# Performance work log

Measured on AMD Instinct MI355X. Metric: run time of the kernel, lower is better.

## Reference

```python
import jax, jax.numpy as jnp
import numpy as np

CUTOFF = 5.0
NUM_RBF = 8
POLY_P = 5
AVG_NEIGH = 16.0
NUM_LAYERS = 2
NUM_RANKS = 4  # edge angular ranks 0..3 (Cartesian dims 1,3,9,27)
C = 64


def _radial(edge_vec):
    # r: [E,1]; Bessel-j0 basis with polynomial cutoff envelope (MACE-style)
    r = jnp.sqrt(jnp.sum(edge_vec * edge_vec, axis=-1, keepdims=True) + 1e-12)
    x = r / CUTOFF
    p = float(POLY_P)
    env = (1.0 - 0.5 * (p + 1.0) * (p + 2.0) * x**POLY_P
           + p * (p + 2.0) * x**(POLY_P + 1)
           - 0.5 * p * (p + 1.0) * x**(POLY_P + 2))
    env = jnp.where(x < 1.0, env, 0.0)
    k = jnp.arange(1, NUM_RBF + 1, dtype=edge_vec.dtype)
    basis = jnp.sqrt(2.0 / CUTOFF) * jnp.sin(k * jnp.pi * x) / r  # [E,K]
    return basis * env, r


def _angular(rhat):
    # Cartesian ICTD-style angular basis, ranks 0..3, norm constants sqrt(2r+1)
    E = rhat.shape[0]
    y0 = jnp.ones((E, 1), rhat.dtype)
    y1 = jnp.sqrt(3.0) * rhat  # [E,3]
    o2 = rhat[:, :, None] * rhat[:, None, :]
    y2 = jnp.sqrt(5.0) * o2.reshape(E, 9)
    o3 = o2[:, :, :, None] * rhat[:, None, None, :]
    y3 = jnp.sqrt(7.0) * o3.reshape(E, 27)
    return (y0, y1, y2, y3)


def setup_inputs() -> dict:
    key = jax.random.key(0)
    ks = jax.random.split(key, 12)
    N, E = 5000, 80000
    species = jax.random.randint(ks[0], (N,), 0, 10, dtype=jnp.int32)
    senders = jax.random.randint(ks[1], (E,), 0, N, dtype=jnp.int32)
    receivers = jax.random.randint(ks[2], (E,), 0, N, dtype=jnp.int32)
    edge_vec = 1.5 * jax.random.normal(ks[3], (E, 3), jnp.float32)
    embed_w = jax.random.normal(ks[4], (10, C), jnp.float32)
    rad_w1 = jax.random.normal(ks[5], (NUM_LAYERS, NUM_RBF, 64), jnp.float32) / np.sqrt(NUM_RBF)
    rad_w2 = jax.random.normal(ks[6], (NUM_LAYERS, 64, 64), jnp.float32) / 8.0
    rad_w3 = jax.random.normal(ks[7], (NUM_LAYERS, 64, 64), jnp.float32) / 8.0
    rad_w4 = jax.random.normal(ks[8], (NUM_LAYERS, 64, NUM_RANKS * C), jnp.float32) / 8.0
    mix_w = jax.random.normal(ks[9], (NUM_LAYERS, NUM_RANKS, C, C), jnp.float32) / 8.0
    read_w = jax.random.normal(ks[10], (NUM_LAYERS, C), jnp.float32) / 8.0
    return {"species": species, "senders": senders, "receivers": receivers,
            "edge_vec": edge_vec, "embed_w": embed_w, "rad_w1": rad_w1,
            "rad_w2": rad_w2, "rad_w3": rad_w3, "rad_w4": rad_w4,
            "mix_w": mix_w, "read_w": read_w}


def reference(species, senders, receivers, edge_vec, embed_w,
              rad_w1, rad_w2, rad_w3, rad_w4, mix_w, read_w):
    N = species.shape[0]
    E = edge_vec.shape[0]
    rb, r = _radial(edge_vec)                      # [E,K]
    rhat = edge_vec / r
    Y = _angular(rhat)                             # tuple of [E,dim_r]
    h0 = embed_w[species]                          # [N,C] species embedding
    node_energy = jnp.zeros((N,), edge_vec.dtype)
    for l in range(NUM_LAYERS):
        # radial MLP -> per-rank, per-channel edge weights [E, NUM_RANKS, C]
        h = jax.nn.silu(rb @ rad_w1[l])
        h = jax.nn.silu(h @ rad_w2[l])
        h = jax.nn.silu(h @ rad_w3[l])
        R = (h @ rad_w4[l]).reshape(E, NUM_RANKS, C)
        hj = h0[senders]                           # neighbor gather [E,C]
        h0_new = jnp.zeros_like(h0)
        for ri in range(NUM_RANKS):
            # equivariant edge tensor product: radial * scalar feat x angular
            m = (R[:, ri, :] * hj)[:, :, None] * Y[ri][:, None, :]  # [E,C,dim]
            A = jax.ops.segment_sum(m, receivers, num_segments=N) / AVG_NEIGH
            if ri == 0:
                h0_new = h0_new + A[..., 0] @ mix_w[l, 0]
            else:
                # correlation-2 invariant contraction of equivariant features
                h0_new = h0_new + jnp.einsum('ncd,ncd->nc', A, A) @ mix_w[l, ri]
        node_energy = node_energy + h0_new @ read_w[l]
        h0 = h0_new
    return node_energy
```

## Files before the change

kernel.cpp:

```cpp
#include <hip/hip_runtime.h>
#include <math.h>


#define PI_F 3.14159265358979323846f
#define LOG2E_F 1.44269504088896340736f

typedef _Float16 f16x8 __attribute__((ext_vector_type(8)));
typedef _Float16 f16x2 __attribute__((ext_vector_type(2)));
typedef float f32x4 __attribute__((ext_vector_type(4)));

union FU { uint4 u; f16x8 h; };

__device__ __forceinline__ float silu_f(float x) {
    float e = __builtin_amdgcn_exp2f(-LOG2E_F * x);
    return x * __builtin_amdgcn_rcpf(1.0f + e);
}

__device__ __forceinline__ uint pack2_f16(float a, float b) {
    return __builtin_bit_cast(uint, __builtin_amdgcn_cvt_pkrtz(a, b));
}

__device__ __forceinline__ float unpk_f16(uint u, int hi) {
    unsigned short s = hi ? (unsigned short)(u >> 16) : (unsigned short)(u & 0xffff);
    return (float)__builtin_bit_cast(_Float16, s);
}

__global__ void k_edge_basis(const float* __restrict__ ev,
                             const int* __restrict__ recv,
                             uint*  __restrict__ rbh,
                             float* __restrict__ rhat4,
                             int*   __restrict__ counts,
                             int E)
{
    int e = blockIdx.x * blockDim.x + threadIdx.x;
    if (e >= E) return;
    float vx = ev[3*e+0], vy = ev[3*e+1], vz = ev[3*e+2];
    float r2 = vx*vx + vy*vy + vz*vz + 1e-12f;
    float r  = sqrtf(r2);
    float x  = r * 0.2f;
    float x2 = x*x;
    float x5 = x2*x2*x;
    float env = 1.0f + x5*(-21.0f + x*(35.0f - 15.0f*x));
    if (x >= 1.0f) env = 0.0f;
    float pref = 0.632455532033675866f / r * env;
    float pix  = PI_F * x;
    float bas[8];
    #pragma unroll
    for (int k = 0; k < 8; ++k) bas[k] = pref * __sinf((float)(k+1) * pix);
    uint* o = rbh + (size_t)e*4;
    #pragma unroll
    for (int k = 0; k < 4; ++k) o[k] = pack2_f16(bas[2*k], bas[2*k+1]);

    float ir = 1.0f / r;
    float4 rh;
    rh.x = vx*ir; rh.y = vy*ir; rh.z = vz*ir; rh.w = 0.0f;
    *(float4*)(rhat4 + (size_t)e*4) = rh;

    atomicAdd(&counts[recv[e]], 1);
}

__global__ void k_scan(const int* __restrict__ counts, int* __restrict__ offsets, int N)
{
    __shared__ int wsum[16];
    __shared__ int basev;
    int lane = threadIdx.x & 63;
    int w    = threadIdx.x >> 6;
    if (threadIdx.x == 0) basev = 0;
    __syncthreads();
    for (int start = 0; start < N; start += 1024) {
        int i = start + (int)threadIdx.x;
        int v = (i < N) ? counts[i] : 0;
        int s = v;
        #pragma unroll
        for (int off = 1; off < 64; off <<= 1) {
            int t = __shfl_up(s, off, 64);
            if (lane >= off) s += t;
        }
        if (lane == 63) wsum[w] = s;
        __syncthreads();
        int wbase = 0;
        {
            int ws = (lane < 16) ? wsum[lane] : 0;
            #pragma unroll
            for (int off = 1; off < 16; off <<= 1) {
                int t = __shfl_up(ws, off, 64);
                if (lane >= off) ws += t;
            }
            int excl = __shfl(ws, w - 1, 64);
            wbase = (w == 0) ? 0 : excl;
        }
        if (i < N) offsets[i] = basev + wbase + s - v;
        __syncthreads();
        if (threadIdx.x == 1023) basev += wbase + s;
        __syncthreads();
    }
    if (threadIdx.x == 0) offsets[N] = basev;
}

__global__ void k_scatter(const int* __restrict__ recv,
                          const int* __restrict__ offsets,
                          int* __restrict__ cursor,
                          int* __restrict__ elist, int E)
{
    int e = blockIdx.x * blockDim.x + threadIdx.x;
    if (e >= E) return;
    int r = recv[e];
    int p = atomicAdd(&cursor[r], 1);
    elist[offsets[r] + p] = e;
}

__global__ __launch_bounds__(256) void k_sort_wave(
    const int* __restrict__ offsets, int* __restrict__ elist, int N)
{
    int lane = threadIdx.x & 63;
    int node = (blockIdx.x * blockDim.x + threadIdx.x) >> 6;
    if (node >= N) return;
    int beg = offsets[node], end = offsets[node+1];
    int d = end - beg;
    if (d <= 1) return;
    if (d <= 64) {
        int v = (lane < d) ? elist[beg + lane] : 0x7fffffff;
        int rank = 0;
        #pragma unroll 8
        for (int j = 0; j < 64; ++j) {
            int vj = __shfl(v, j, 64);
            rank += (vj < v) ? 1 : 0;
        }
        if (lane < d) elist[beg + rank] = v;
    } else {
        if (lane == 0) {
            for (int i = beg + 1; i < end; ++i) {
                int v = elist[i];
                int j = i - 1;
                while (j >= beg && elist[j] > v) { elist[j+1] = elist[j]; --j; }
                elist[j+1] = v;
            }
        }
    }
}

__global__ void k_embed(const int* __restrict__ species,
                        const float* __restrict__ embw,
                        float* __restrict__ h0, int NC)
{
    int i = blockIdx.x * blockDim.x + threadIdx.x;
    if (i >= NC) return;
    int n = i >> 6, c = i & 63;
    h0[i] = embw[species[n]*64 + c];
}

__global__ void k_prep_w(const float* __restrict__ rw1,
                         const float* __restrict__ rw2,
                         const float* __restrict__ rw3,
                         const float* __restrict__ rw4,
                         uint* __restrict__ Wf1, uint* __restrict__ Wf2,
                         uint* __restrict__ Wf3, uint* __restrict__ Wf4)
{
    int tid = blockIdx.x * blockDim.x + threadIdx.x;
    if (tid < 2048) {
        int reg = tid & 3, lane = (tid >> 2) & 63, ot = (tid >> 8) & 3, l = tid >> 10;
        int out = 16*ot + (lane & 15);
        int k   = 8*(lane >> 4) + 2*reg;
        float lo = (k   < 8) ? rw1[l*512 + k*64 + out]     : 0.0f;
        float hi = (k+1 < 8) ? rw1[l*512 + (k+1)*64 + out] : 0.0f;
        Wf1[tid] = pack2_f16(lo, hi);
        return;
    }
    int t = tid - 2048;
    if (t < 4096) {
        int reg = t & 3, lane = (t >> 2) & 63, kt = (t >> 8) & 1, ot = (t >> 9) & 3, l = t >> 11;
        int out = 16*ot + (lane & 15);
        int k   = 32*kt + 8*(lane >> 4) + 2*reg;
        Wf2[t] = pack2_f16(rw2[l*4096 + k*64 + out], rw2[l*4096 + (k+1)*64 + out]);
        return;
    }
    t -= 4096;
    if (t < 4096) {
        int reg = t & 3, lane = (t >> 2) & 63, kt = (t >> 8) & 1, ot = (t >> 9) & 3, l = t >> 11;
        int out = 16*ot + (lane & 15);
        int k   = 32*kt + 8*(lane >> 4) + 2*reg;
        Wf3[t] = pack2_f16(rw3[l*4096 + k*64 + out], rw3[l*4096 + (k+1)*64 + out]);
        return;
    }
    t -= 4096;
    if (t < 16384) {
        int reg = t & 3, lane = (t >> 2) & 63, kt = (t >> 8) & 1, ot = (t >> 9) & 15, l = t >> 13;
        int out = 16*ot + (lane & 15);
        int k   = 32*kt + 8*(lane >> 4) + 2*reg;
        Wf4[t] = pack2_f16(rw4[l*16384 + k*256 + out], rw4[l*16384 + (k+1)*256 + out]);
    }
}

__global__ __launch_bounds__(256) void k_mlp_mfma(
    const uint* __restrict__ rbh,
    const uint* __restrict__ Wf1, const uint* __restrict__ Wf2,
    const uint* __restrict__ Wf3, const uint* __restrict__ Wf4,
    uint* __restrict__ Rpk,
    int E, int tiles)
{
    __shared__ __align__(16) uint Hl[4][16][132];
    int lane = threadIdx.x & 63;
    int w    = threadIdx.x >> 6;
    int wid  = blockIdx.x * 4 + w;
    if (wid >= 2 * tiles) return;
    int l    = wid / tiles;
    int tile = wid % tiles;
    int e0   = tile * 16;

    uint (*H)[132] = Hl[w];
    int er = lane & 15;
    int kb = lane >> 4;

    f32x4 zero4 = {0.f, 0.f, 0.f, 0.f};

    FU b;
    if (kb == 0) {
        int e = e0 + er;
        if (e < E) b.u = *(const uint4*)(rbh + (size_t)e*4);
        else       b.u = make_uint4(0,0,0,0);
    } else {
        b.u = make_uint4(0,0,0,0);
    }
    f32x4 d[4];
    #pragma unroll
    for (int ot = 0; ot < 4; ++ot) {
        FU a;
        a.u = *(const uint4*)(Wf1 + ((size_t)(l*4 + ot)*64 + lane)*4);
        d[ot] = __builtin_amdgcn_mfma_f32_16x16x32_f16(a.h, b.h, zero4, 0, 0, 0);
    }
    #pragma unroll
    for (int ot = 0; ot < 4; ++ot) {
        uint p0 = pack2_f16(silu_f(d[ot][0]), silu_f(d[ot][1]));
        uint p1 = pack2_f16(silu_f(d[ot][2]), silu_f(d[ot][3]));
        uint* dst = &H[er][8*ot + 2*kb];
        dst[0] = p0; dst[1] = p1;
    }

    const uint* Wfs[2] = { Wf2, Wf3 };
    #pragma unroll
    for (int s = 0; s < 2; ++s) {
        FU hb0, hb1;
        hb0.u = *(const uint4*)&H[er][4*kb];
        hb1.u = *(const uint4*)&H[er][16 + 4*kb];
        #pragma unroll
        for (int ot = 0; ot < 4; ++ot) {
            FU a;
            a.u = *(const uint4*)(Wfs[s] + ((size_t)((l*4 + ot)*2 + 0)*64 + lane)*4);
            d[ot] = __builtin_amdgcn_mfma_f32_16x16x32_f16(a.h, hb0.h, zero4, 0, 0, 0);
            a.u = *(const uint4*)(Wfs[s] + ((size_t)((l*4 + ot)*2 + 1)*64 + lane)*4);
            d[ot] = __builtin_amdgcn_mfma_f32_16x16x32_f16(a.h, hb1.h, d[ot], 0, 0, 0);
        }
        #pragma unroll
        for (int ot = 0; ot < 4; ++ot) {
            uint p0 = pack2_f16(silu_f(d[ot][0]), silu_f(d[ot][1]));
            uint p1 = pack2_f16(silu_f(d[ot][2]), silu_f(d[ot][3]));
            uint* dst = &H[er][8*ot + 2*kb];
            dst[0] = p0; dst[1] = p1;
        }
    }

    FU hb0, hb1;
    hb0.u = *(const uint4*)&H[er][4*kb];
    hb1.u = *(const uint4*)&H[er][16 + 4*kb];
    #pragma unroll
    for (int ri = 0; ri < 4; ++ri) {
        #pragma unroll
        for (int otl = 0; otl < 4; ++otl) {
            int ot = ri*4 + otl;
            FU a;
            f32x4 d2;
            a.u = *(const uint4*)(Wf4 + ((size_t)((l*16 + ot)*2 + 0)*64 + lane)*4);
            d2 = __builtin_amdgcn_mfma_f32_16x16x32_f16(a.h, hb0.h, zero4, 0, 0, 0);
            a.u = *(const uint4*)(Wf4 + ((size_t)((l*16 + ot)*2 + 1)*64 + lane)*4);
            d2 = __builtin_amdgcn_mfma_f32_16x16x32_f16(a.h, hb1.h, d2, 0, 0, 0);
            int p = otl*8 + kb*2;
            H[er][(p  )*4 + ri] = pack2_f16(d2[0], d2[1]);
            H[er][(p+1)*4 + ri] = pack2_f16(d2[2], d2[3]);
        }
    }
    #pragma unroll
    for (int it = 0; it < 8; ++it) {
        int f   = it*64 + lane;
        int row = f >> 5;
        int q4  = (f & 31) * 4;
        int eg  = e0 + row;
        if (eg < E)
            *(uint4*)(Rpk + ((size_t)l*E + eg)*128 + q4) = *(const uint4*)&H[row][q4];
    }
}

__global__ __launch_bounds__(256) void k_node(
    const uint*  __restrict__ Rpk,
    const float* __restrict__ h0,
    const int*   __restrict__ senders,
    const float* __restrict__ rhat4,
    const int*   __restrict__ offsets,
    const int*   __restrict__ elist,
    const float* __restrict__ mixw,
    const float* __restrict__ readw,
    float* __restrict__ h0n,
    const float* __restrict__ eprev,
    float* __restrict__ eout,
    int N)
{
    int gtid = blockIdx.x * blockDim.x + threadIdx.x;
    int wave = gtid >> 6;
    int lane = threadIdx.x & 63;
    int w    = threadIdx.x >> 6;
    __shared__ float Bl[4][4][64];
    bool active = (wave < N);
    int n = active ? wave : 0;
    int half  = lane & 1;
    int cpair = lane >> 1;

    float a0 = 0.f;
    float a1[3]  = {0.f,0.f,0.f};
    float a2[6]  = {0.f,0.f,0.f,0.f,0.f,0.f};
    float a3[10] = {0.f,0.f,0.f,0.f,0.f,0.f,0.f,0.f,0.f,0.f};

    auto accum = [&](float x, float y, float z, float hj, uint4 qv) {
        float t0 = unpk_f16(qv.x, half) * hj;
        float t1 = unpk_f16(qv.y, half) * hj;
        float t2 = unpk_f16(qv.z, half) * hj;
        float t3 = unpk_f16(qv.w, half) * hj;
        a0 += t0;
        a1[0] = fmaf(t1, x, a1[0]);
        a1[1] = fmaf(t1, y, a1[1]);
        a1[2] = fmaf(t1, z, a1[2]);
        float qxx = x*x, qxy = x*y, qxz = x*z, qyy = y*y, qyz = y*z, qzz = z*z;
        a2[0] = fmaf(t2, qxx, a2[0]);
        a2[1] = fmaf(t2, qxy, a2[1]);
        a2[2] = fmaf(t2, qxz, a2[2]);
        a2[3] = fmaf(t2, qyy, a2[3]);
        a2[4] = fmaf(t2, qyz, a2[4]);
        a2[5] = fmaf(t2, qzz, a2[5]);
        float u0 = t3*qxx, u1 = t3*qxy, u3 = t3*qyy, u5 = t3*qzz;
        a3[0] = fmaf(u0, x, a3[0]);
        a3[1] = fmaf(u0, y, a3[1]);
        a3[2] = fmaf(u0, z, a3[2]);
        a3[3] = fmaf(u3, x, a3[3]);
        a3[4] = fmaf(u1, z, a3[4]);
        a3[5] = fmaf(u5, x, a3[5]);
        a3[6] = fmaf(u3, y, a3[6]);
        a3[7] = fmaf(u3, z, a3[7]);
        a3[8] = fmaf(u5, y, a3[8]);
        a3[9] = fmaf(u5, z, a3[9]);
    };

    if (active) {
        int beg = __builtin_amdgcn_readfirstlane(offsets[n]);
        int end = __builtin_amdgcn_readfirstlane(offsets[n+1]);
        int i = beg;
        for (; i + 4 <= end; i += 4) {
            int   e_[4], sn_[4];
            #pragma unroll
            for (int k = 0; k < 4; ++k) {
                e_[k]  = __builtin_amdgcn_readfirstlane(elist[i+k]);
                sn_[k] = __builtin_amdgcn_readfirstlane(senders[e_[k]]);
            }
            float4 rh_[4]; float hj_[4]; uint4 q_[4];
            #pragma unroll
            for (int k = 0; k < 4; ++k) {
                rh_[k] = *(const float4*)(rhat4 + (size_t)e_[k]*4);
                hj_[k] = h0[(size_t)sn_[k]*64 + lane];
                q_[k]  = *(const uint4*)(Rpk + (size_t)e_[k]*128 + cpair*4);
            }
            #pragma unroll
            for (int k = 0; k < 4; ++k)
                accum(rh_[k].x, rh_[k].y, rh_[k].z, hj_[k], q_[k]);
        }
        for (; i < end; ++i) {
            int e   = __builtin_amdgcn_readfirstlane(elist[i]);
            int snd = __builtin_amdgcn_readfirstlane(senders[e]);
            float4 rh = *(const float4*)(rhat4 + (size_t)e*4);
            float  hj = h0[(size_t)snd*64 + lane];
            uint4  qv = *(const uint4*)(Rpk + (size_t)e*128 + cpair*4);
            accum(rh.x, rh.y, rh.z, hj, qv);
        }
    }

    float B0 = a0 * 0.0625f;
    float s1 = a1[0]*a1[0] + a1[1]*a1[1] + a1[2]*a1[2];
    float B1 = s1 * (3.0f/256.0f);
    float s2 = a2[0]*a2[0] + a2[3]*a2[3] + a2[5]*a2[5]
             + 2.0f*(a2[1]*a2[1] + a2[2]*a2[2] + a2[4]*a2[4]);
    float B2 = s2 * (5.0f/256.0f);
    float s3 = a3[0]*a3[0] + a3[6]*a3[6] + a3[9]*a3[9]
             + 3.0f*(a3[1]*a3[1] + a3[2]*a3[2] + a3[3]*a3[3]
                   + a3[5]*a3[5] + a3[7]*a3[7] + a3[8]*a3[8])
             + 6.0f*a3[4]*a3[4];
    float B3 = s3 * (7.0f/256.0f);

    Bl[w][0][lane] = B0;
    Bl[w][1][lane] = B1;
    Bl[w][2][lane] = B2;
    Bl[w][3][lane] = B3;
    __syncthreads();

    if (active) {
        float acc = 0.0f;
        for (int ri = 0; ri < 4; ++ri) {
            #pragma unroll 8
            for (int j = 0; j < 64; ++j)
                acc = fmaf(Bl[w][ri][j], mixw[(ri*64 + j)*64 + lane], acc);
        }
        h0n[(size_t)n*64 + lane] = acc;

        float evl = acc * readw[lane];
        #pragma unroll
        for (int off = 1; off < 64; off <<= 1) evl += __shfl_xor(evl, off, 64);
        if (lane == 0) {
            float o = evl;
            if (eprev) o += eprev[n];
            eout[n] = o;
        }
    }
}

extern "C" void kernel_launch(void* const* d_in, const int* in_sizes, int n_in,
                              void* d_out, int out_size, void* d_ws, size_t ws_size,
                              hipStream_t stream)
{
    const int*   species   = (const int*)  d_in[0];
    const int*   senders   = (const int*)  d_in[1];
    const int*   receivers = (const int*)  d_in[2];
    const float* edge_vec  = (const float*)d_in[3];
    const float* embed_w   = (const float*)d_in[4];
    const float* rad_w1    = (const float*)d_in[5];
    const float* rad_w2    = (const float*)d_in[6];
    const float* rad_w3    = (const float*)d_in[7];
    const float* rad_w4    = (const float*)d_in[8];
    const float* mix_w     = (const float*)d_in[9];
    const float* read_w    = (const float*)d_in[10];

    int N = in_sizes[0];
    int E = in_sizes[1];
    float* out = (float*)d_out;

    char* ws = (char*)d_ws;
    size_t off = 0;
    auto alloc = [&](size_t bytes) -> char* {
        char* p = ws + off;
        off = (off + bytes + 255) & ~(size_t)255;
        return p;
    };
    uint*  rbh   = (uint*) alloc((size_t)E*4*sizeof(uint));
    float* rhat4 = (float*)alloc((size_t)E*4*sizeof(float));
    float* h0a   = (float*)alloc((size_t)N*64*sizeof(float));
    float* h0b   = (float*)alloc((size_t)N*64*sizeof(float));
    float* ener  = (float*)alloc((size_t)N*sizeof(float));
    int* counts  = (int*)alloc((size_t)N*sizeof(int));
    int* offsets = (int*)alloc((size_t)(N+1)*sizeof(int));
    int* cursor  = (int*)alloc((size_t)N*sizeof(int));
    int* elist   = (int*)alloc((size_t)E*sizeof(int));
    uint* Wf1    = (uint*)alloc(2048*sizeof(uint));
    uint* Wf2    = (uint*)alloc(4096*sizeof(uint));
    uint* Wf3    = (uint*)alloc(4096*sizeof(uint));
    uint* Wf4    = (uint*)alloc(16384*sizeof(uint));
    uint* Rpk    = (uint*)alloc((size_t)2*E*128*sizeof(uint));

    hipMemsetAsync(counts, 0, (size_t)N*sizeof(int), stream);
    hipMemsetAsync(cursor, 0, (size_t)N*sizeof(int), stream);

    k_edge_basis<<<(E + 255)/256, 256, 0, stream>>>(
        edge_vec, receivers, rbh, rhat4, counts, E);
    k_prep_w<<<(26624 + 255)/256, 256, 0, stream>>>(
        rad_w1, rad_w2, rad_w3, rad_w4, Wf1, Wf2, Wf3, Wf4);
    k_scan<<<1, 1024, 0, stream>>>(counts, offsets, N);
    k_scatter<<<(E + 255)/256, 256, 0, stream>>>(receivers, offsets, cursor, elist, E);
    k_sort_wave<<<((size_t)N*64 + 255)/256, 256, 0, stream>>>(offsets, elist, N);
    k_embed<<<((size_t)N*64 + 255)/256, 256, 0, stream>>>(species, embed_w, h0a, N*64);

    int tiles = (E + 15) / 16;
    int waves = 2 * tiles;
    k_mlp_mfma<<<(waves + 3)/4, 256, 0, stream>>>(
        rbh, Wf1, Wf2, Wf3, Wf4, Rpk, E, tiles);

    float* hcur = h0a;
    float* hnxt = h0b;
    for (int l = 0; l < 2; ++l) {
        uint* Rl = Rpk + (size_t)l * E * 128;
        k_node<<<((size_t)N*64 + 255)/256, 256, 0, stream>>>(
            Rl, hcur, senders, rhat4, offsets, elist,
            mix_w + (size_t)l*4*64*64,
            read_w + (size_t)l*64,
            hnxt,
            (l == 0) ? nullptr : ener,
            (l == 0) ? ener : out,
            N);
        float* tmp = hcur; hcur = hnxt; hnxt = tmp;
    }
}
```

Baseline: 118.4 us.

## Fuse setup kernels and double-buffer edge gathers in node aggregation loop

Merges the two memsets, the weight-prep kernel and the embedding kernel into a single setup launch, removing three launches and their dispatch gaps. In the node kernel, the 4-edge batch loop becomes a ping-pong double buffer that issues the next batch's gathers (elist, senders, rhat, h0, R) before accumulating the current one. This hides gather latency but roughly doubles the live registers for the load buffers, which could reduce occupancy.

```diff
diff --git a/kernel.cpp b/kernel.cpp
--- a/kernel.cpp
+++ b/kernel.cpp
@@ -6,7 +6,6 @@
 #define LOG2E_F 1.44269504088896340736f
 
 typedef _Float16 f16x8 __attribute__((ext_vector_type(8)));
-typedef _Float16 f16x2 __attribute__((ext_vector_type(2)));
 typedef float f32x4 __attribute__((ext_vector_type(4)));
 
 union FU { uint4 u; f16x8 h; };
@@ -23,6 +22,55 @@
 __device__ __forceinline__ float unpk_f16(uint u, int hi) {
     unsigned short s = hi ? (unsigned short)(u >> 16) : (unsigned short)(u & 0xffff);
     return (float)__builtin_bit_cast(_Float16, s);
+}
+
+__global__ void k_setup(const float* __restrict__ rw1,
+                        const float* __restrict__ rw2,
+                        const float* __restrict__ rw3,
+                        const float* __restrict__ rw4,
+                        uint* __restrict__ Wf1, uint* __restrict__ Wf2,
+                        uint* __restrict__ Wf3, uint* __restrict__ Wf4,
+                        const int* __restrict__ species,
+                        const float* __restrict__ embw,
+                        float* __restrict__ h0,
+                        int* __restrict__ counts, int* __restrict__ cursor,
+                        int N, int NC)
+{
+    int tid = blockIdx.x * blockDim.x + threadIdx.x;
+    if (tid < N) { counts[tid] = 0; cursor[tid] = 0; }
+    if (tid < NC) {
+        int n = tid >> 6, c = tid & 63;
+        h0[tid] = embw[species[n]*64 + c];
+    }
+    if (tid < 2048) {
+        int reg = tid & 3, lane = (tid >> 2) & 63, ot = (tid >> 8) & 3, l = tid >> 10;
+        int out = 16*ot + (lane & 15);
+        int k   = 8*(lane >> 4) + 2*reg;
+        float lo = (k   < 8) ? rw1[l*512 + k*64 + out]     : 0.0f;
+        float hi = (k+1 < 8) ? rw1[l*512 + (k+1)*64 + out] : 0.0f;
+        Wf1[tid] = pack2_f16(lo, hi);
+    }
+    if (tid >= 2048 && tid < 2048 + 4096) {
+        int t = tid - 2048;
+        int reg = t & 3, lane = (t >> 2) & 63, kt = (t >> 8) & 1, ot = (t >> 9) & 3, l = t >> 11;
+        int out = 16*ot + (lane & 15);
+        int k   = 32*kt + 8*(lane >> 4) + 2*reg;
+        Wf2[t] = pack2_f16(rw2[l*4096 + k*64 + out], rw2[l*4096 + (k+1)*64 + out]);
+    }
+    if (tid >= 6144 && tid < 6144 + 4096) {
+        int t = tid - 6144;
+        int reg = t & 3, lane = (t >> 2) & 63, kt = (t >> 8) & 1, ot = (t >> 9) & 3, l = t >> 11;
+        int out = 16*ot + (lane & 15);
+        int k   = 32*kt + 8*(lane >> 4) + 2*reg;
+        Wf3[t] = pack2_f16(rw3[l*4096 + k*64 + out], rw3[l*4096 + (k+1)*64 + out]);
+    }
+    if (tid >= 10240 && tid < 10240 + 16384) {
+        int t = tid - 10240;
+        int reg = t & 3, lane = (t >> 2) & 63, kt = (t >> 8) & 1, ot = (t >> 9) & 15, l = t >> 13;
+        int out = 16*ot + (lane & 15);
+        int k   = 32*kt + 8*(lane >> 4) + 2*reg;
+        Wf4[t] = pack2_f16(rw4[l*16384 + k*256 + out], rw4[l*16384 + (k+1)*256 + out]);
+    }
 }
 
 __global__ void k_edge_basis(const float* __restrict__ ev,
@@ -136,58 +184,6 @@
                 elist[j+1] = v;
             }
         }
-    }
-}
-
-__global__ void k_embed(const int* __restrict__ species,
-                        const float* __restrict__ embw,
-                        float* __restrict__ h0, int NC)
-{
-    int i = blockIdx.x * blockDim.x + threadIdx.x;
-    if (i >= NC) return;
-    int n = i >> 6, c = i & 63;
-    h0[i] = embw[species[n]*64 + c];
-}
-
-__global__ void k_prep_w(const float* __restrict__ rw1,
-                         const float* __restrict__ rw2,
-                         const float* __restrict__ rw3,
-                         const float* __restrict__ rw4,
-                         uint* __restrict__ Wf1, uint* __restrict__ Wf2,
-                         uint* __restrict__ Wf3, uint* __restrict__ Wf4)
-{
-    int tid = blockIdx.x * blockDim.x + threadIdx.x;
-    if (tid < 2048) {
-        int reg = tid & 3, lane = (tid >> 2) & 63, ot = (tid >> 8) & 3, l = tid >> 10;
-        int out = 16*ot + (lane & 15);
-        int k   = 8*(lane >> 4) + 2*reg;
-        float lo = (k   < 8) ? rw1[l*512 + k*64 + out]     : 0.0f;
-        float hi = (k+1 < 8) ? rw1[l*512 + (k+1)*64 + out] : 0.0f;
-        Wf1[tid] = pack2_f16(lo, hi);
-        return;
-    }
-    int t = tid - 2048;
-    if (t < 4096) {
-        int reg = t & 3, lane = (t >> 2) & 63, kt = (t >> 8) & 1, ot = (t >> 9) & 3, l = t >> 11;
-        int out = 16*ot + (lane & 15);
-        int k   = 32*kt + 8*(lane >> 4) + 2*reg;
-        Wf2[t] = pack2_f16(rw2[l*4096 + k*64 + out], rw2[l*4096 + (k+1)*64 + out]);
-        return;
-    }
-    t -= 4096;
-    if (t < 4096) {
-        int reg = t & 3, lane = (t >> 2) & 63, kt = (t >> 8) & 1, ot = (t >> 9) & 3, l = t >> 11;
-        int out = 16*ot + (lane & 15);
-        int k   = 32*kt + 8*(lane >> 4) + 2*reg;
-        Wf3[t] = pack2_f16(rw3[l*4096 + k*64 + out], rw3[l*4096 + (k+1)*64 + out]);
-        return;
-    }
-    t -= 4096;
-    if (t < 16384) {
-        int reg = t & 3, lane = (t >> 2) & 63, kt = (t >> 8) & 1, ot = (t >> 9) & 15, l = t >> 13;
-        int out = 16*ot + (lane & 15);
-        int k   = 32*kt + 8*(lane >> 4) + 2*reg;
-        Wf4[t] = pack2_f16(rw4[l*16384 + k*256 + out], rw4[l*16384 + (k+1)*256 + out]);
     }
 }
 
@@ -351,23 +347,54 @@
         int beg = __builtin_amdgcn_readfirstlane(offsets[n]);
         int end = __builtin_amdgcn_readfirstlane(offsets[n+1]);
         int i = beg;
-        for (; i + 4 <= end; i += 4) {
-            int   e_[4], sn_[4];
+        int nfull = (end - beg) >> 2;
+
+        int eA[4], snA[4]; float4 rhA[4]; float hjA[4]; uint4 qA[4];
+        int eB[4], snB[4]; float4 rhB[4]; float hjB[4]; uint4 qB[4];
+
+        auto loadb = [&](int ii, int (&e_)[4], int (&sn_)[4],
+                         float4 (&rh_)[4], float (&hj_)[4], uint4 (&q_)[4]) {
             #pragma unroll
             for (int k = 0; k < 4; ++k) {
-                e_[k]  = __builtin_amdgcn_readfirstlane(elist[i+k]);
+                e_[k]  = __builtin_amdgcn_readfirstlane(elist[ii+k]);
                 sn_[k] = __builtin_amdgcn_readfirstlane(senders[e_[k]]);
             }
-            float4 rh_[4]; float hj_[4]; uint4 q_[4];
             #pragma unroll
             for (int k = 0; k < 4; ++k) {
                 rh_[k] = *(const float4*)(rhat4 + (size_t)e_[k]*4);
                 hj_[k] = h0[(size_t)sn_[k]*64 + lane];
                 q_[k]  = *(const uint4*)(Rpk + (size_t)e_[k]*128 + cpair*4);
             }
+        };
+        auto accumb = [&](float4 (&rh_)[4], float (&hj_)[4], uint4 (&q_)[4]) {
             #pragma unroll
             for (int k = 0; k < 4; ++k)
                 accum(rh_[k].x, rh_[k].y, rh_[k].z, hj_[k], q_[k]);
+        };
+
+        if (nfull > 0) {
+            loadb(i, eA, snA, rhA, hjA, qA);
+            int b = 0;
+            for (;;) {
+                if (b + 1 < nfull) {
+                    loadb(i + 4, eB, snB, rhB, hjB, qB);
+                    accumb(rhA, hjA, qA);
+                    ++b; i += 4;
+                    if (b + 1 < nfull) {
+                        loadb(i + 4, eA, snA, rhA, hjA, qA);
+                        accumb(rhB, hjB, qB);
+                        ++b; i += 4;
+                    } else {
+                        accumb(rhB, hjB, qB);
+                        ++b; i += 4;
+                        break;
+                    }
+                } else {
+                    accumb(rhA, hjA, qA);
+                    ++b; i += 4;
+                    break;
+                }
+            }
         }
         for (; i < end; ++i) {
             int e   = __builtin_amdgcn_readfirstlane(elist[i]);
@@ -459,17 +486,16 @@
     uint* Wf4    = (uint*)alloc(16384*sizeof(uint));
     uint* Rpk    = (uint*)alloc((size_t)2*E*128*sizeof(uint));
 
-    hipMemsetAsync(counts, 0, (size_t)N*sizeof(int), stream);
-    hipMemsetAsync(cursor, 0, (size_t)N*sizeof(int), stream);
+    int NC = N * 64;
+    k_setup<<<(NC + 255)/256, 256, 0, stream>>>(
+        rad_w1, rad_w2, rad_w3, rad_w4, Wf1, Wf2, Wf3, Wf4,
+        species, embed_w, h0a, counts, cursor, N, NC);
 
     k_edge_basis<<<(E + 255)/256, 256, 0, stream>>>(
         edge_vec, receivers, rbh, rhat4, counts, E);
-    k_prep_w<<<(26624 + 255)/256, 256, 0, stream>>>(
-        rad_w1, rad_w2, rad_w3, rad_w4, Wf1, Wf2, Wf3, Wf4);
     k_scan<<<1, 1024, 0, stream>>>(counts, offsets, N);
     k_scatter<<<(E + 255)/256, 256, 0, stream>>>(receivers, offsets, cursor, elist, E);
     k_sort_wave<<<((size_t)N*64 + 255)/256, 256, 0, stream>>>(offsets, elist, N);
-    k_embed<<<((size_t)N*64 + 255)/256, 256, 0, stream>>>(species, embed_w, h0a, N*64);
 
     int tiles = (E + 15) / 16;
     int waves = 2 * tiles;
```

Result: slower. 128.0 us (+8.1%).
